# Kernel optimization log

Hardware: AMD Instinct MI355X
Metric: run time of the kernel (lower is better)

Reference implementation:

```python
import jax, jax.numpy as jnp
import numpy as np

EPS = 1e-6
B, T, D = 8, 4096, 512


def setup_inputs() -> dict:
    key = jax.random.key(0)
    ks = jax.random.split(key, 8)
    s = 1.0 / np.sqrt(D)
    return {
        "summarization": jax.random.normal(ks[0], (B, D), jnp.float32),
        "decoder_output": jax.random.normal(ks[1], (B, T, D), jnp.float32),
        "W_hist": jax.random.normal(ks[2], (D, D), jnp.float32) * s,
        "b_hist": jnp.zeros((D,), jnp.float32),
        "W1": jax.random.normal(ks[3], (D, D), jnp.float32) * s,
        "W2": jax.random.normal(ks[4], (D, D), jnp.float32) * s,
        "W_out": jax.random.normal(ks[5], (D, D), jnp.float32) * s,
        "b_out": jnp.zeros((D,), jnp.float32),
        "gamma": jnp.ones((D,), jnp.float32),
        "beta": jnp.zeros((D,), jnp.float32),
    }


def reference(summarization, decoder_output, W_hist, b_hist, W1, W2, W_out, b_out, gamma, beta):
    # Causal running mean: equivalent to tril-mask bmm / row-count, but O(T).
    tgt_len = decoder_output.shape[1]
    counts = jnp.arange(1, tgt_len + 1, dtype=decoder_output.dtype)[None, :, None]
    history = jnp.cumsum(decoder_output, axis=1) / counts            # [B,T,D]
    history = jnp.tanh(history @ W_hist + b_hist)                    # history_linear + tanh
    # TransformMinus: linear1(summ) - linear2(history), then linear_out + tanh
    summ_proj = (summarization @ W1)[:, None, :]                     # [B,1,D] broadcasts over T
    out = summ_proj - history @ W2
    future = jnp.tanh(out @ W_out + b_out)
    # LayerPostprocessing (eval: dropout = identity): LayerNorm(future + decoder_output)
    x = future + decoder_output
    mu = jnp.mean(x, axis=-1, keepdims=True)
    var = jnp.mean(jnp.square(x - mu), axis=-1, keepdims=True)
    return (x - mu) / jnp.sqrt(var + EPS) * gamma + beta
```

## Files before the change

### kernel.cpp

```cpp
#include <hip/hip_runtime.h>
#include <hip/hip_bf16.h>
#include <stdint.h>
#include <stddef.h>

#define DEV static __device__ __forceinline__

typedef __attribute__((ext_vector_type(8))) short short8;
typedef __attribute__((ext_vector_type(4))) float floatx4;

constexpr int Tn = 4096, Dn = 512;
constexpr int NC = 128, CTm = 32;

union U8s { uint4 u4; unsigned short us[8]; };
union U4f { float4 f4; float f[4]; };
union U4s { uint2 u2; unsigned short us[4]; };

DEV float b2f(unsigned short u) {
  union { unsigned int i; float f; } c; c.i = ((unsigned int)u) << 16; return c.f;
}
DEV unsigned short f2b(float f) {
  union { float f; unsigned int u; } c; c.f = f;
  unsigned int r = c.u + 0x7fffu + ((c.u >> 16) & 1u);
  return (unsigned short)(r >> 16);
}
DEV float fast_tanh(float x) {
  float e = __expf(2.0f * x);
  return 1.0f - 2.0f / (e + 1.0f);
}

typedef __attribute__((address_space(1))) void GVOID;
typedef __attribute__((address_space(3))) void LVOID;
DEV void async16(const unsigned short* g, unsigned short* l) {
  __builtin_amdgcn_global_load_lds((GVOID*)g, (LVOID*)l, 16, 0, 0);
}

__global__ void k_scan_partial(const float* __restrict__ dec, float* __restrict__ part) {
  int idx = blockIdx.x * 256 + threadIdx.x;
  int d4 = idx & 127;
  int c  = (idx >> 7) & (NC - 1);
  int b  = idx >> 14;
  const float* p = dec + ((size_t)b * Tn + (size_t)c * CTm) * Dn + d4 * 4;
  float s[4] = {0,0,0,0};
#pragma unroll 4
  for (int i = 0; i < CTm; ++i) {
    U4f v; v.f4 = *(const float4*)(p + (size_t)i * Dn);
#pragma unroll
    for (int j = 0; j < 4; ++j) s[j] += v.f[j];
  }
  float* o = part + ((size_t)(b * NC + c)) * Dn + d4 * 4;
#pragma unroll
  for (int j = 0; j < 4; ++j) o[j] = s[j];
}

__global__ void k_scan_apply(const float* __restrict__ dec,
                             const float* __restrict__ part,
                             unsigned short* __restrict__ M) {
  int idx = blockIdx.x * 256 + threadIdx.x;
  int d8 = idx & 63;
  int c  = (idx >> 6) & (NC - 1);
  int b  = idx >> 13;
  size_t rbase = (size_t)b * Tn + (size_t)c * CTm;
  float s[8] = {0,0,0,0,0,0,0,0};
  const float* pb = part + (size_t)b * NC * Dn + d8 * 8;
  for (int cc = 0; cc < c; ++cc) {
    U4f p0, p1;
    p0.f4 = *(const float4*)(pb + (size_t)cc * Dn);
    p1.f4 = *(const float4*)(pb + (size_t)cc * Dn + 4);
#pragma unroll
    for (int j = 0; j < 4; ++j) { s[j] += p0.f[j]; s[j + 4] += p1.f[j]; }
  }
  int t0 = c * CTm;
  for (int i = 0; i < CTm; ++i) {
    U4f v0, v1; U8s o;
    v0.f4 = *(const float4*)(dec + (rbase + i) * Dn + d8 * 8);
    v1.f4 = *(const float4*)(dec + (rbase + i) * Dn + d8 * 8 + 4);
    float inv = 1.0f / (float)(t0 + i + 1);
#pragma unroll
    for (int j = 0; j < 4; ++j) {
      s[j] += v0.f[j];     o.us[j]     = f2b(s[j] * inv);
      s[j + 4] += v1.f[j]; o.us[j + 4] = f2b(s[j + 4] * inv);
    }
    *(uint4*)(M + (rbase + i) * Dn + d8 * 8) = o.u4;
  }
}

__global__ void k_svec(const float* __restrict__ summ,
                       const unsigned short* __restrict__ W1WoT,
                       const float* __restrict__ bo,
                       float* __restrict__ spo) {
  int widx = blockIdx.x * 4 + (threadIdx.x >> 6);
  int lane = threadIdx.x & 63;
  int n = widx & 511; int b = widx >> 9;
  U8s w8; w8.u4 = *(const uint4*)(W1WoT + (size_t)n * Dn + lane * 8);
  U4f s0, s1;
  s0.f4 = *(const float4*)(summ + (size_t)b * Dn + lane * 8);
  s1.f4 = *(const float4*)(summ + (size_t)b * Dn + lane * 8 + 4);
  float acc = 0.f;
#pragma unroll
  for (int j = 0; j < 4; ++j) acc += s0.f[j] * b2f(w8.us[j]);
#pragma unroll
  for (int j = 0; j < 4; ++j) acc += s1.f[j] * b2f(w8.us[j + 4]);
#pragma unroll
  for (int o = 32; o > 0; o >>= 1) acc += __shfl_xor(acc, o, 64);
  if (lane == 0) spo[(size_t)b * Dn + n] = acc + bo[n];
}

__global__ void k_wprep(const float* __restrict__ Wh, const float* __restrict__ Wo,
                        const float* __restrict__ W1, const float* __restrict__ W2,
                        unsigned short* __restrict__ WhT, unsigned short* __restrict__ WoT,
                        unsigned short* __restrict__ W1b, unsigned short* __restrict__ W2b) {
  int blk = blockIdx.x;
  if (blk < 128) {
    const float* in = (blk < 64) ? Wh : Wo;
    unsigned short* out = (blk < 64) ? WhT : WoT;
    int lb = blk & 63;
    __shared__ float t[64][65];
    int n0 = (lb & 7) * 64, k0 = (lb >> 3) * 64;
#pragma unroll
    for (int l = 0; l < 16; ++l) {
      int lin = l * 256 + threadIdx.x;
      int r = lin >> 6, c = lin & 63;
      t[r][c] = in[(size_t)(k0 + r) * 512 + n0 + c];
    }
    __syncthreads();
#pragma unroll
    for (int l = 0; l < 16; ++l) {
      int lin = l * 256 + threadIdx.x;
      int r = lin >> 6, c = lin & 63;
      out[(size_t)(n0 + r) * 512 + k0 + c] = f2b(t[c][r]);
    }
  } else {
    const float* in = (blk < 160) ? W1 : W2;
    unsigned short* out = (blk < 160) ? W1b : W2b;
    int lb = (blk - 128) & 31;
    size_t base = ((size_t)lb * 256 + threadIdx.x) * 32;
#pragma unroll
    for (int l = 0; l < 8; ++l) {
      U4f v; v.f4 = *(const float4*)(in + base + l * 4);
      U4s o;
#pragma unroll
      for (int j = 0; j < 4; ++j) o.us[j] = f2b(v.f[j]);
      *(uint2*)(out + base + l * 4) = o.u2;
    }
  }
}

template<int EPI>
DEV void gemm_core(const unsigned short* __restrict__ A, const unsigned short* __restrict__ BT,
                   unsigned short* __restrict__ C, const float* __restrict__ bias,
                   const float* __restrict__ sproj, int m0, int n0) {
  __shared__ alignas(16) unsigned short sA[128 * 64];
  __shared__ alignas(16) unsigned short sB[128 * 64];
  const int tid  = threadIdx.x;
  const int lane = tid & 63;
  const int w    = tid >> 6;
  const int wm   = (w >> 1) * 64;
  const int wn   = (w & 1) * 64;
  const int rs   = lane & 15;
  const int quad = lane >> 4;

  floatx4 acc[4][4];
#pragma unroll
  for (int i = 0; i < 4; ++i)
#pragma unroll
    for (int j = 0; j < 4; ++j) acc[i][j] = (floatx4){0.f, 0.f, 0.f, 0.f};

  for (int kt = 0; kt < 512; kt += 64) {
#pragma unroll
    for (int l = 0; l < 4; ++l) {
      int ch = l * 256 + tid;
      int r = ch >> 3, kc = ch & 7;
      async16(A  + (size_t)(m0 + r) * 512 + kt + kc * 8, sA + (size_t)ch * 8);
      async16(BT + (size_t)(n0 + r) * 512 + kt + kc * 8, sB + (size_t)ch * 8);
    }
    asm volatile("s_waitcnt vmcnt(0)" ::: "memory");
    __syncthreads();

#pragma unroll
    for (int kk = 0; kk < 2; ++kk) {
      const int kb = kk * 32 + quad * 8;
      short8 af[4], bfr[4];
#pragma unroll
      for (int i = 0; i < 4; ++i)
        af[i] = *(const short8*)(sA + (size_t)(wm + i * 16 + rs) * 64 + kb);
#pragma unroll
      for (int j = 0; j < 4; ++j)
        bfr[j] = *(const short8*)(sB + (size_t)(wn + j * 16 + rs) * 64 + kb);
#pragma unroll
      for (int i = 0; i < 4; ++i)
#pragma unroll
        for (int j = 0; j < 4; ++j)
          acc[i][j] = __builtin_amdgcn_mfma_f32_16x16x32_bf16(af[i], bfr[j], acc[i][j], 0, 0, 0);
    }
    __syncthreads();
  }

#pragma unroll
  for (int i = 0; i < 4; ++i) {
#pragma unroll
    for (int j = 0; j < 4; ++j) {
      const int colg = n0 + wn + j * 16 + rs;
#pragma unroll
      for (int r = 0; r < 4; ++r) {
        const int rowg = m0 + wm + i * 16 + quad * 4 + r;
        float v = acc[i][j][r];
        if constexpr (EPI == 0)      v = fast_tanh(v + bias[colg]);
        else if constexpr (EPI == 3) v = fast_tanh(sproj[(rowg >> 12) * Dn + colg] - v);
        C[(size_t)rowg * 512 + colg] = f2b(v);
      }
    }
  }
}

template<int EPI>
__global__ __launch_bounds__(256, 2)
void k_gemm(const unsigned short* __restrict__ A, const unsigned short* __restrict__ BT,
            unsigned short* __restrict__ C, const float* __restrict__ bias,
            const float* __restrict__ sproj) {
  gemm_core<EPI>(A, BT, C, bias, sproj, blockIdx.x * 128, blockIdx.y * 128);
}

__global__ __launch_bounds__(256, 2)
void k_wgemm(const unsigned short* __restrict__ WoT,
             const unsigned short* __restrict__ W2b, const unsigned short* __restrict__ W1b,
             unsigned short* __restrict__ W2WoT, unsigned short* __restrict__ W1WoT) {
  const unsigned short* BT = blockIdx.z ? W1b : W2b;
  unsigned short* C = blockIdx.z ? W1WoT : W2WoT;
  gemm_core<2>(WoT, BT, C, nullptr, nullptr, blockIdx.x * 128, blockIdx.y * 128);
}

__global__ void k_ln(const unsigned short* __restrict__ F, const float* __restrict__ dec,
                     const float* __restrict__ gamma, const float* __restrict__ beta,
                     float* __restrict__ out) {
  int row  = blockIdx.x * 4 + (threadIdx.x >> 6);
  int lane = threadIdx.x & 63;
  size_t base = (size_t)row * Dn + lane * 8;
  U8s f8; f8.u4 = *(const uint4*)(F + base);
  U4f d0, d1; d0.f4 = *(const float4*)(dec + base); d1.f4 = *(const float4*)(dec + base + 4);
  float x[8]; float s = 0.f, sq = 0.f;
#pragma unroll
  for (int j = 0; j < 8; ++j) {
    float dv = (j < 4) ? d0.f[j] : d1.f[j - 4];
    x[j] = b2f(f8.us[j]) + dv; s += x[j]; sq += x[j] * x[j];
  }
#pragma unroll
  for (int o = 32; o > 0; o >>= 1) { s += __shfl_xor(s, o, 64); sq += __shfl_xor(sq, o, 64); }
  float mu   = s * (1.0f / 512.0f);
  float var  = sq * (1.0f / 512.0f) - mu * mu;
  float rstd = rsqrtf(var + 1e-6f);
  U4f g0, g1, b0, b1, o0, o1;
  g0.f4 = *(const float4*)(gamma + lane * 8); g1.f4 = *(const float4*)(gamma + lane * 8 + 4);
  b0.f4 = *(const float4*)(beta  + lane * 8); b1.f4 = *(const float4*)(beta  + lane * 8 + 4);
#pragma unroll
  for (int j = 0; j < 8; ++j) {
    float g = (j < 4) ? g0.f[j] : g1.f[j - 4];
    float b = (j < 4) ? b0.f[j] : b1.f[j - 4];
    float v = (x[j] - mu) * rstd * g + b;
    if (j < 4) o0.f[j] = v; else o1.f[j - 4] = v;
  }
  *(float4*)(out + base) = o0.f4;
  *(float4*)(out + base + 4) = o1.f4;
}

extern "C" void kernel_launch(void* const* d_in, const int* in_sizes, int n_in,
                              void* d_out, int out_size, void* d_ws, size_t ws_size,
                              hipStream_t stream) {
  (void)in_sizes; (void)n_in; (void)out_size; (void)ws_size;
  const float* summ = (const float*)d_in[0];
  const float* dec  = (const float*)d_in[1];
  const float* Wh   = (const float*)d_in[2];
  const float* bh   = (const float*)d_in[3];
  const float* W1   = (const float*)d_in[4];
  const float* W2   = (const float*)d_in[5];
  const float* Wo   = (const float*)d_in[6];
  const float* bo   = (const float*)d_in[7];
  const float* gam  = (const float*)d_in[8];
  const float* bet  = (const float*)d_in[9];
  float* out = (float*)d_out;

  char* ws = (char*)d_ws;
  unsigned short* Mbuf  = (unsigned short*)(ws);
  unsigned short* Hbuf  = (unsigned short*)(ws + 33554432);
  float*          part  = (float*)(ws + 67108864);
  float*          spo   = (float*)(ws + 69206016);
  unsigned short* WhT   = (unsigned short*)(ws + 69238784);
  unsigned short* WoT   = (unsigned short*)(ws + 69763072);
  unsigned short* W2b   = (unsigned short*)(ws + 70287360);
  unsigned short* W2WoT = (unsigned short*)(ws + 70811648);
  unsigned short* W1b   = (unsigned short*)(ws + 71335936);
  unsigned short* W1WoT = (unsigned short*)(ws + 71860224);

  k_scan_partial<<<512, 256, 0, stream>>>(dec, part);

  k_wprep<<<192, 256, 0, stream>>>(Wh, Wo, W1, W2, WhT, WoT, W1b, W2b);
  k_wgemm<<<dim3(4, 4, 2), 256, 0, stream>>>(WoT, W2b, W1b, W2WoT, W1WoT);

  k_svec<<<1024, 256, 0, stream>>>(summ, W1WoT, bo, spo);

  k_scan_apply<<<256, 256, 0, stream>>>(dec, part, Mbuf);

  k_gemm<0><<<dim3(256, 4), 256, 0, stream>>>(Mbuf, WhT, Hbuf, bh, nullptr);
  k_gemm<3><<<dim3(256, 4), 256, 0, stream>>>(Hbuf, W2WoT, Mbuf, nullptr, spo);

  k_ln<<<8192, 256, 0, stream>>>(Mbuf, dec, gam, bet, out);
}
```

Baseline: 262.8 us.

## Precompute exclusive chunk prefix sums in wprep and widen scan_apply parallelism

Adds four extra blocks to the weight-prep kernel that turn the per-chunk partial sums into exclusive prefix sums in place. scan_apply then loads a single prefix vector per chunk instead of re-summing up to 127 earlier chunk partials per thread, which was quadratic redundant work. scan_apply also switches to 4 features per thread with twice as many blocks to raise occupancy. The prefix pass runs serially over 128 chunks per column, but that work is tiny and overlaps the weight preparation.

```diff
diff --git a/kernel.cpp b/kernel.cpp
--- a/kernel.cpp
+++ b/kernel.cpp
@@ -56,31 +56,22 @@
                              const float* __restrict__ part,
                              unsigned short* __restrict__ M) {
   int idx = blockIdx.x * 256 + threadIdx.x;
-  int d8 = idx & 63;
-  int c  = (idx >> 6) & (NC - 1);
-  int b  = idx >> 13;
+  int d4 = idx & 127;
+  int c  = (idx >> 7) & (NC - 1);
+  int b  = idx >> 14;
   size_t rbase = (size_t)b * Tn + (size_t)c * CTm;
-  float s[8] = {0,0,0,0,0,0,0,0};
-  const float* pb = part + (size_t)b * NC * Dn + d8 * 8;
-  for (int cc = 0; cc < c; ++cc) {
-    U4f p0, p1;
-    p0.f4 = *(const float4*)(pb + (size_t)cc * Dn);
-    p1.f4 = *(const float4*)(pb + (size_t)cc * Dn + 4);
-#pragma unroll
-    for (int j = 0; j < 4; ++j) { s[j] += p0.f[j]; s[j + 4] += p1.f[j]; }
-  }
+  U4f s; s.f4 = *(const float4*)(part + ((size_t)b * NC + c) * Dn + d4 * 4);
   int t0 = c * CTm;
+  const float* dp = dec + rbase * Dn + d4 * 4;
+  unsigned short* mp = M + rbase * Dn + d4 * 4;
+#pragma unroll 4
   for (int i = 0; i < CTm; ++i) {
-    U4f v0, v1; U8s o;
-    v0.f4 = *(const float4*)(dec + (rbase + i) * Dn + d8 * 8);
-    v1.f4 = *(const float4*)(dec + (rbase + i) * Dn + d8 * 8 + 4);
+    U4f v; v.f4 = *(const float4*)(dp + (size_t)i * Dn);
     float inv = 1.0f / (float)(t0 + i + 1);
-#pragma unroll
-    for (int j = 0; j < 4; ++j) {
-      s[j] += v0.f[j];     o.us[j]     = f2b(s[j] * inv);
-      s[j + 4] += v1.f[j]; o.us[j + 4] = f2b(s[j + 4] * inv);
-    }
-    *(uint4*)(M + (rbase + i) * Dn + d8 * 8) = o.u4;
+    U4s o;
+#pragma unroll
+    for (int j = 0; j < 4; ++j) { s.f[j] += v.f[j]; o.us[j] = f2b(s.f[j] * inv); }
+    *(uint2*)(mp + (size_t)i * Dn) = o.u2;
   }
 }
 
@@ -108,7 +99,8 @@
 __global__ void k_wprep(const float* __restrict__ Wh, const float* __restrict__ Wo,
                         const float* __restrict__ W1, const float* __restrict__ W2,
                         unsigned short* __restrict__ WhT, unsigned short* __restrict__ WoT,
-                        unsigned short* __restrict__ W1b, unsigned short* __restrict__ W2b) {
+                        unsigned short* __restrict__ W1b, unsigned short* __restrict__ W2b,
+                        float* __restrict__ part) {
   int blk = blockIdx.x;
   if (blk < 128) {
     const float* in = (blk < 64) ? Wh : Wo;
@@ -129,7 +121,7 @@
       int r = lin >> 6, c = lin & 63;
       out[(size_t)(n0 + r) * 512 + k0 + c] = f2b(t[c][r]);
     }
-  } else {
+  } else if (blk < 192) {
     const float* in = (blk < 160) ? W1 : W2;
     unsigned short* out = (blk < 160) ? W1b : W2b;
     int lb = (blk - 128) & 31;
@@ -141,6 +133,24 @@
 #pragma unroll
       for (int j = 0; j < 4; ++j) o.us[j] = f2b(v.f[j]);
       *(uint2*)(out + base + l * 4) = o.u2;
+    }
+  } else {
+    int idx = (blk - 192) * 256 + threadIdx.x;
+    int d4 = idx & 127;
+    int b  = idx >> 7;
+    float* p = part + (size_t)b * NC * Dn + d4 * 4;
+    float s[4] = {0, 0, 0, 0};
+    for (int c0 = 0; c0 < NC; c0 += 8) {
+      U4f v[8];
+#pragma unroll
+      for (int i = 0; i < 8; ++i) v[i].f4 = *(const float4*)(p + (size_t)(c0 + i) * Dn);
+#pragma unroll
+      for (int i = 0; i < 8; ++i) {
+        U4f o;
+#pragma unroll
+        for (int j = 0; j < 4; ++j) { o.f[j] = s[j]; s[j] += v[i].f[j]; }
+        *(float4*)(p + (size_t)(c0 + i) * Dn) = o.f4;
+      }
     }
   }
 }
@@ -292,12 +302,12 @@
 
   k_scan_partial<<<512, 256, 0, stream>>>(dec, part);
 
-  k_wprep<<<192, 256, 0, stream>>>(Wh, Wo, W1, W2, WhT, WoT, W1b, W2b);
+  k_wprep<<<196, 256, 0, stream>>>(Wh, Wo, W1, W2, WhT, WoT, W1b, W2b, part);
   k_wgemm<<<dim3(4, 4, 2), 256, 0, stream>>>(WoT, W2b, W1b, W2WoT, W1WoT);
 
   k_svec<<<1024, 256, 0, stream>>>(summ, W1WoT, bo, spo);
 
-  k_scan_apply<<<256, 256, 0, stream>>>(dec, part, Mbuf);
+  k_scan_apply<<<512, 256, 0, stream>>>(dec, part, Mbuf);
 
   k_gemm<0><<<dim3(256, 4), 256, 0, stream>>>(Mbuf, WhT, Hbuf, bh, nullptr);
   k_gemm<3><<<dim3(256, 4), 256, 0, stream>>>(Hbuf, W2WoT, Mbuf, nullptr, spo);
```

Measured after the change: 244.2 us. 1.08x faster.
